# Optimization experiments

Hardware: AMD Instinct MI355X
Metric: run time of the kernel (lower is better)

## Reference

```python
import jax, jax.numpy as jnp
import numpy as np

B, S, HID = 1, 1024, 4096
NH, NKV, HD = 32, 8, 128
GROUPS = NH // NKV
THETA = 10000.0
SPAR = 0.5          # sparse_aggression (layer_idx > 0)
MIN_IDX = 4         # min_sparse_index: always-kept sink tokens
NEG = jnp.float32(-1e30)


def setup_inputs() -> dict:
    key = jax.random.key(0)
    k0, k1, k2, k3, k4 = jax.random.split(key, 5)
    sc = 0.02
    return {
        "hidden_states": jax.random.normal(k0, (B, S, HID), jnp.float32),
        "position_ids": jnp.arange(S, dtype=jnp.int32)[None, :],
        "Wq": jax.random.normal(k1, (NH * HD, HID), jnp.float32) * sc,
        "Wk": jax.random.normal(k2, (NKV * HD, HID), jnp.float32) * sc,
        "Wv": jax.random.normal(k3, (NKV * HD, HID), jnp.float32) * sc,
        "Wo": jax.random.normal(k4, (HID, NH * HD), jnp.float32) * sc,
    }


def _rotate_half(x):
    h = x.shape[-1] // 2
    return jnp.concatenate([-x[..., h:], x[..., :h]], axis=-1)


def _rope_cos_sin(position_ids):
    inv_freq = 1.0 / (THETA ** (jnp.arange(0, HD, 2, dtype=jnp.float32) / HD))
    freqs = position_ids.astype(jnp.float32)[..., None] * inv_freq  # [B,S,HD/2]
    emb = jnp.concatenate([freqs, freqs], axis=-1)                  # [B,S,HD]
    return jnp.cos(emb)[:, None], jnp.sin(emb)[:, None]             # [B,1,S,HD]


def reference(hidden_states, position_ids, Wq, Wk, Wv, Wo):
    b, s, _ = hidden_states.shape
    # QKV projections (nn.Linear: x @ W.T)
    q = (hidden_states @ Wq.T).reshape(b, s, NH, HD).transpose(0, 2, 1, 3)
    k = (hidden_states @ Wk.T).reshape(b, s, NKV, HD).transpose(0, 2, 1, 3)
    v = (hidden_states @ Wv.T).reshape(b, s, NKV, HD).transpose(0, 2, 1, 3)
    # RoPE
    cos, sin = _rope_cos_sin(position_ids)
    q = q * cos + _rotate_half(q) * sin
    k = k * cos + _rotate_half(k) * sin
    # repeat_kv (GQA expansion)
    k = jnp.repeat(k, GROUPS, axis=1)
    v = jnp.repeat(v, GROUPS, axis=1)
    # causal additive mask [1,1,S,S]
    causal = jnp.where(jnp.triu(jnp.ones((s, s), bool), 1), NEG, jnp.float32(0))[None, None]
    scale = 1.0 / np.sqrt(HD)
    scores = jnp.einsum('bhqd,bhkd->bhqk', q, k) * scale
    # oracle importance: softmax of (softmaxed) masked attention (no_grad in original)
    oracle = jax.nn.softmax((scores + causal).astype(jnp.float32), axis=-1)
    importance = jax.nn.softmax(oracle, axis=-1)
    importance = jax.lax.stop_gradient(importance)
    # descending sort -> rank of each key for each query
    sorted_idx = jnp.argsort(-importance, axis=-1)          # [B,H,S,S]
    ranks = jnp.argsort(sorted_idx, axis=-1)                # inverse perm
    # per-query token budget: keep ceil-ish top-k proportional to row length
    k_per_row = jnp.maximum((SPAR * (jnp.arange(s) + 1)).astype(jnp.int32), 1)
    key_idx = jnp.arange(s)
    kept = (ranks < k_per_row[None, None, :, None]) | (key_idx[None, None, None, :] < MIN_IDX)
    sparse_mask = jnp.where(kept, jnp.float32(0), NEG)
    # sparse attention
    attn = scores + sparse_mask + causal
    probs = jax.nn.softmax(attn.astype(jnp.float32), axis=-1).astype(v.dtype)
    out = jnp.einsum('bhqk,bhkd->bhqd', probs, v)           # [B,H,S,HD]
    out = out.transpose(0, 2, 1, 3).reshape(b, s, NH * HD)
    return out @ Wo.T
```

## Files before the change

kernel.cpp:

```cpp
#include <hip/hip_runtime.h>
#include <hip/hip_bf16.h>

#define S_LEN 1024
#define HID   4096
#define NH    32
#define NKV   8
#define HD    128
#define MIN_IDX 4
#define AO_COLS 4096
#define HEAD_STRIDE 131072

typedef __attribute__((ext_vector_type(8))) short short8;
typedef __attribute__((ext_vector_type(4))) float f32x4;

__device__ __forceinline__ unsigned short f2bf(float f) {
  union { float f; unsigned u; } v; v.f = f;
  unsigned r = v.u + 0x7FFFu + ((v.u >> 16) & 1u);
  return (unsigned short)(r >> 16);
}
__device__ __forceinline__ float bf2f(unsigned short h) {
  union { unsigned u; float f; } v; v.u = ((unsigned)h) << 16;
  return v.f;
}
__device__ __forceinline__ unsigned pk2(float a, float b) {
  union { __hip_bfloat162 h; unsigned u; } c;
  c.h = __float22bfloat162_rn(make_float2(a, b));
  return c.u;
}
__device__ __forceinline__ short8 pack8(float4 a, float4 b) {
  union { short8 s; unsigned u[4]; } r;
  r.u[0] = pk2(a.x, a.y); r.u[1] = pk2(a.z, a.w);
  r.u[2] = pk2(b.x, b.y); r.u[3] = pk2(b.z, b.w);
  return r.s;
}
__device__ __forceinline__ unsigned ordf(float f) {
  union { float f; int i; } v; v.f = f;
  return (unsigned)(v.i ^ ((v.i >> 31) | 0x80000000));
}
__device__ __forceinline__ float iordf(unsigned u) {
  union { int i; float f; } v;
  v.i = (u & 0x80000000u) ? (int)(u ^ 0x80000000u) : (int)~u;
  return v.f;
}
__device__ __forceinline__ float wave_sum_f(float v) {
  #pragma unroll
  for (int m = 32; m >= 1; m >>= 1) v += __shfl_xor(v, m);
  return v;
}
__device__ __forceinline__ unsigned wave_max_u(unsigned v) {
  #pragma unroll
  for (int m = 32; m >= 1; m >>= 1) { unsigned o = __shfl_xor(v, m); v = o > v ? o : v; }
  return v;
}
__device__ __forceinline__ void wave_lds_fence() {
  __builtin_amdgcn_s_waitcnt(0xC07F);
  __builtin_amdgcn_wave_barrier();
}
__device__ __forceinline__ void gload_lds16(const unsigned short* g, unsigned short* l) {
  auto gp = (const __attribute__((address_space(1))) unsigned*)g;
  auto lp = (__attribute__((address_space(3))) unsigned*)(unsigned)(unsigned long long)l;
  __builtin_amdgcn_global_load_lds(gp, lp, 16, 0, 0);
}

__global__ __launch_bounds__(256) void cvt4_k(
    const float* __restrict__ s0, const float* __restrict__ s1,
    const float* __restrict__ s2, const float* __restrict__ s3,
    unsigned short* __restrict__ d0, unsigned short* __restrict__ d1)
{
  const int b = blockIdx.x;
  const float* src; unsigned short* dst; int rb;
  if (b < 2048)       { src = s0; dst = d0;            rb = b; }
  else if (b < 10240) { src = s1; dst = d1;            rb = b - 2048; }
  else if (b < 12288) { src = s2; dst = d1 + 16777216; rb = b - 10240; }
  else                { src = s3; dst = d1 + 20971520; rb = b - 12288; }
  const size_t i = ((size_t)rb * 256 + threadIdx.x) * 8;
  float4 a = *(const float4*)(src + i);
  float4 c = *(const float4*)(src + i + 4);
  *(short8*)(dst + i) = pack8(a, c);
}

__global__ __launch_bounds__(256) void gemm_qkv_k(
    const unsigned short* __restrict__ Xb, const unsigned short* __restrict__ Wb,
    unsigned short* __restrict__ Qraw, unsigned short* __restrict__ Vt)
{
  __shared__ unsigned short As[3][128 * 32];
  __shared__ unsigned short Bs[3][128 * 32];
  const int nt = blockIdx.x;
  const int n0 = nt * 128;
  const int m0 = blockIdx.y * 128;
  const int t = threadIdx.x, w = t >> 6, lane = t & 63;
  const int wm = w >> 1, wn = w & 1;
  const int mcol = lane & 15, quad = lane >> 4;
  const int lrow = lane >> 2, lcol = (lane & 3) * 8;

  const unsigned short* Ag = Xb + (size_t)m0 * HID;
  const unsigned short* Bg = Wb + (size_t)n0 * HID;

  f32x4 acc[4][4];
  #pragma unroll
  for (int i = 0; i < 4; i++)
    #pragma unroll
    for (int j = 0; j < 4; j++) acc[i][j] = (f32x4){0.f, 0.f, 0.f, 0.f};

  constexpr int NT = HID / 32;
  #define STAGE_QKV(buf, k0)                                                  \
    { const int c0 = w * 2, c1 = w * 2 + 1;                                   \
      gload_lds16(Ag + (size_t)(c0*16 + lrow) * HID + (k0) + lcol, &As[buf][c0 * 512]); \
      gload_lds16(Bg + (size_t)(c0*16 + lrow) * HID + (k0) + lcol, &Bs[buf][c0 * 512]); \
      gload_lds16(Ag + (size_t)(c1*16 + lrow) * HID + (k0) + lcol, &As[buf][c1 * 512]); \
      gload_lds16(Bg + (size_t)(c1*16 + lrow) * HID + (k0) + lcol, &Bs[buf][c1 * 512]); }

  STAGE_QKV(0, 0)
  STAGE_QKV(1, 32)
  asm volatile("s_waitcnt vmcnt(4)" ::: "memory");
  __builtin_amdgcn_s_barrier();
  __builtin_amdgcn_sched_barrier(0);

  int cur = 0, stg = 2;
  for (int kt = 0; kt < NT; ++kt) {
    if (kt + 2 < NT) STAGE_QKV(stg, (kt + 2) * 32)
    short8 af[4], bf[4];
    #pragma unroll
    for (int i = 0; i < 4; i++) af[i] = *(const short8*)&As[cur][(wm*64 + i*16 + mcol)*32 + quad*8];
    #pragma unroll
    for (int j = 0; j < 4; j++) bf[j] = *(const short8*)&Bs[cur][(wn*64 + j*16 + mcol)*32 + quad*8];
    #pragma unroll
    for (int i = 0; i < 4; i++)
      #pragma unroll
      for (int j = 0; j < 4; j++)
        acc[i][j] = __builtin_amdgcn_mfma_f32_16x16x32_bf16(af[i], bf[j], acc[i][j], 0, 0, 0);
    if (kt + 2 < NT) { asm volatile("s_waitcnt vmcnt(4)" ::: "memory"); }
    else             { asm volatile("s_waitcnt vmcnt(0)" ::: "memory"); }
    __builtin_amdgcn_s_barrier();
    __builtin_amdgcn_sched_barrier(0);
    cur = (cur == 2) ? 0 : cur + 1;
    stg = (stg == 2) ? 0 : stg + 1;
  }

  if (nt < 40) {
    unsigned short* dst = Qraw + (size_t)nt * HEAD_STRIDE;
    #pragma unroll
    for (int i = 0; i < 4; i++) {
      const int rb = m0 + wm*64 + i*16 + quad*4;
      #pragma unroll
      for (int j = 0; j < 4; j++) {
        const int d = wn*64 + j*16 + mcol;
        #pragma unroll
        for (int r = 0; r < 4; r++)
          dst[(size_t)(rb + r) * HD + d] = f2bf(acc[i][j][r]);
      }
    }
  } else {
    unsigned short* dst = Vt + (size_t)(nt - 40) * HEAD_STRIDE;
    #pragma unroll
    for (int i = 0; i < 4; i++) {
      const int rb = m0 + wm*64 + i*16 + quad*4;
      #pragma unroll
      for (int j = 0; j < 4; j++) {
        const int d = wn*64 + j*16 + mcol;
        ushort4 v4;
        v4.x = f2bf(acc[i][j][0]); v4.y = f2bf(acc[i][j][1]);
        v4.z = f2bf(acc[i][j][2]); v4.w = f2bf(acc[i][j][3]);
        *(ushort4*)(dst + (size_t)d * S_LEN + rb) = v4;
      }
    }
  }
}

__global__ __launch_bounds__(256) void rope_qk_k(
    const int* __restrict__ pos_ids, unsigned short* __restrict__ Qraw)
{
  const int w = threadIdx.x >> 6, lane = threadIdx.x & 63;
  const int gw = blockIdx.x * 4 + w;
  const int hidx = gw >> 10;
  const int s = gw & 1023;
  const float pos = (float)pos_ids[s];
  const float invf = exp2f((float)lane * -0.20762050593045f);
  float sn, cs;
  sincosf(pos * invf, &sn, &cs);
  unsigned short* base = Qraw + (size_t)hidx * HEAD_STRIDE + (size_t)s * HD;
  const float x0 = bf2f(base[lane]), x1 = bf2f(base[lane + 64]);
  base[lane]      = f2bf(x0 * cs - x1 * sn);
  base[lane + 64] = f2bf(x1 * cs + x0 * sn);
}

#define SROW 1042
#define PSTR 2084

#define PROC_ROW(UARR, RR, LL, PRE, PM, KRM, TTT)                             \
  {                                                                           \
    const int r_ = (RR);                                                      \
    const int L_ = (LL);                                                      \
    unsigned btau = (PRE);                                                    \
    unsigned bmsk = (PM);                                                     \
    int kr = (KRM);                                                           \
    int tt = (TTT);                                                           \
    const int bs = (bmsk == 0u) ? 31 : (__builtin_ctz(bmsk) - 1);             \
    _Pragma("unroll 1")                                                       \
    for (int b = bs; b >= 0; --b) {                                           \
      if (tt <= kr) break;                                                    \
      const unsigned bit = 1u << b;                                           \
      const unsigned am = bmsk | bit;                                         \
      const unsigned test = btau | bit;                                       \
      int cnt = 0;                                                            \
      _Pragma("unroll")                                                       \
      for (int c = 0; c < NC; c++) {                                          \
        const int j = c * 64 + lane;                                          \
        cnt += (int)__popcll(__ballot(j < L_ && ((UARR)[c] & am) == test));   \
      }                                                                       \
      if (cnt >= kr) { btau = test; tt = cnt; }                               \
      else           { kr -= cnt; tt -= cnt; }                                \
      bmsk = am;                                                              \
    }                                                                         \
    unsigned um = 0;                                                          \
    _Pragma("unroll")                                                         \
    for (int c = 0; c < NC; c++) {                                            \
      const int j = c * 64 + lane;                                            \
      if (j < L_ && (UARR)[c] > um) um = (UARR)[c];                           \
    }                                                                         \
    const float mx = iordf(wave_max_u(um));                                   \
    float ssum = 0.f;                                                         \
    if (tt <= kr) {                                                           \
           \
      _Pragma("unroll")                                                       \
      for (int c = 0; c < NC; c++) {                                          \
        const int j = c * 64 + lane;                                          \
        const unsigned u = (UARR)[c];                                         \
        const bool kept = (j < L_) && ((u >= btau) || (j < MIN_IDX));         \
        const float e = kept ? __expf(iordf(u) - mx) : 0.f;                   \
        Pl[r_][c*64 + lane] = f2bf(e);                                        \
        ssum += e;                                                            \
      }                                                                       \
    } else {                                                                  \
      int tiebase = 0;                                                        \
      _Pragma("unroll")                                                       \
      for (int c = 0; c < NC; c++) {                                          \
        const int j = c * 64 + lane;                                          \
        const unsigned u = (UARR)[c];                                         \
        const unsigned umv = u & bmsk;                                        \
        const bool eq = (j < L_) && (umv == btau);                            \
        const unsigned long long bal = __ballot(eq);                          \
        const int trank = tiebase + (int)__popcll(bal & lmlt);                \
        tiebase += (int)__popcll(bal);                                        \
        const bool kept = (j < L_) &&                                         \
            ((umv > btau) || (eq && trank < kr) || (j < MIN_IDX));            \
        const float e = kept ? __expf(iordf(u) - mx) : 0.f;                   \
        Pl[r_][c*64 + lane] = f2bf(e);                                        \
        ssum += e;                                                            \
      }                                                                       \
    }                                                                         \
    ssum = wave_sum_f(ssum);                                                  \
    if (lane == 0) rowinv[r_] = 1.f / fmaxf(ssum, 1e-30f);                    \
  }

template<int KT>
__device__ __forceinline__ void attn_body(
    const unsigned short* __restrict__ Qb, const unsigned short* __restrict__ Kh,
    const unsigned short* __restrict__ Vh, unsigned short* __restrict__ AO,
    float (*S)[SROW], unsigned (*hist)[256], float* rowinv,
    int q0, int h, int w, int lane, int mcol, int quad)
{
  constexpr int NC = 2 * KT;
  const float scale = 0.08838834764831845f;
  unsigned short (*Pl)[PSTR] = (unsigned short (*)[PSTR])&S[0][0];
  const int wk = w & 3, wp = w >> 2;

  short8 aq[4];
  {
    const unsigned short* qrow = Qb + ((size_t)h * S_LEN + q0 + mcol) * HD + quad * 8;
    #pragma unroll
    for (int kk = 0; kk < 4; kk++) aq[kk] = *(const short8*)(qrow + kk * 32);
  }

  #pragma unroll
  for (int kt = wp; kt < KT; kt += 2) {
    short8 bfr[2][4];
    #pragma unroll
    for (int g2 = 0; g2 < 2; g2++) {
      const int key = kt * 128 + (wk * 2 + g2) * 16 + mcol;
      const unsigned short* krow = Kh + (size_t)key * HD + quad * 8;
      #pragma unroll
      for (int kk = 0; kk < 4; kk++) bfr[g2][kk] = *(const short8*)(krow + kk * 32);
    }
    f32x4 d4[2];
    d4[0] = (f32x4){0.f,0.f,0.f,0.f}; d4[1] = (f32x4){0.f,0.f,0.f,0.f};
    #pragma unroll
    for (int g2 = 0; g2 < 2; g2++)
      #pragma unroll
      for (int kk = 0; kk < 4; kk++)
        d4[g2] = __builtin_amdgcn_mfma_f32_16x16x32_bf16(aq[kk], bfr[g2][kk], d4[g2], 0, 0, 0);
    #pragma unroll
    for (int g2 = 0; g2 < 2; g2++) {
      const int ckey = kt * 128 + (wk * 2 + g2) * 16 + mcol;
      #pragma unroll
      for (int r = 0; r < 4; r++) S[quad*4 + r][ckey] = d4[g2][r] * scale;
    }
  }
  __syncthreads();

  const unsigned long long lmlt = (1ull << lane) - 1ull;
  const int rep = lane & 3;
  {
    const int ra = w * 2, rbn = ra + 1;
    const int L0 = q0 + ra + 1, L1 = q0 + rbn + 1;
    unsigned u0[NC], u1[NC];
    #pragma unroll
    for (int c = 0; c < NC; c++) {
      u0[c] = ordf(S[ra][c*64 + lane]);
      u1[c] = ordf(S[rbn][c*64 + lane]);
    }
    int ks0 = L0 >> 1; if (ks0 < 1) ks0 = 1;
    int ks1 = L1 >> 1; if (ks1 < 1) ks1 = 1;
    int krem0 = ks0, tot0 = L0, krem1 = ks1, tot1 = L1;
    unsigned pre0 = 0u, pre1 = 0u, pm0 = 0u, pm1 = 0u;

    #pragma unroll
    for (int pass = 0; pass < 3; pass++) {
      const int shift = 26 - pass * 6;
      const bool a0 = tot0 > krem0, a1 = tot1 > krem1;
      if (!a0 && !a1) continue;
      { uint4 z = {0u, 0u, 0u, 0u}; *(uint4*)&hist[w][lane * 4] = z; }
      wave_lds_fence();
      #pragma unroll
      for (int c = 0; c < NC; c++) {
        const int j = c * 64 + lane;
        if (a0 && j < L0 && (u0[c] & pm0) == pre0)
          atomicAdd(&hist[w][((u0[c] >> shift) & 63) * 4 + rep], 1u);
        if (a1 && j < L1 && (u1[c] & pm1) == pre1)
          atomicAdd(&hist[w][((u1[c] >> shift) & 63) * 4 + rep], 1u << 16);
      }
      wave_lds_fence();
      const uint4 cv = *(const uint4*)&hist[w][(63 - lane) * 4];
      const unsigned cnt2 = cv.x + cv.y + cv.z + cv.w;
      unsigned x = cnt2;
      #pragma unroll
      for (int d2 = 1; d2 < 64; d2 <<= 1) { unsigned y = __shfl_up(x, d2); if (lane >= d2) x += y; }
      const unsigned runp = x - cnt2;
      if (a0) {
        const int run = (int)(runp & 0xFFFFu);
        const int cn  = (int)(cnt2 & 0xFFFFu);
        const bool hit = (run < krem0) && (run + cn >= krem0);
        unsigned packv = hit ? (((unsigned)(63 - lane) << 22) |
                                ((unsigned)run << 11) | (unsigned)cn) : 0u;
        const unsigned long long bal = __ballot(hit);
        const int srcl = __ffsll(bal) - 1;
        const unsigned res = __shfl(packv, srcl);
        krem0 -= (int)((res >> 11) & 0x7FF);
        tot0 = (int)(res & 0x7FF);
        pre0 |= ((unsigned)(res >> 22)) << shift;
        pm0 |= 63u << shift;
      }
      if (a1) {
        const int run = (int)(runp >> 16);
        const int cn  = (int)(cnt2 >> 16);
        const bool hit = (run < krem1) && (run + cn >= krem1);
        unsigned packv = hit ? (((unsigned)(63 - lane) << 22) |
                                ((unsigned)run << 11) | (unsigned)cn) : 0u;
        const unsigned long long bal = __ballot(hit);
        const int srcl = __ffsll(bal) - 1;
        const unsigned res = __shfl(packv, srcl);
        krem1 -= (int)((res >> 11) & 0x7FF);
        tot1 = (int)(res & 0x7FF);
        pre1 |= ((unsigned)(res >> 22)) << shift;
        pm1 |= 63u << shift;
      }
    }
    PROC_ROW(u0, ra,  L0, pre0, pm0, krem0, tot0)
    PROC_ROW(u1, rbn, L1, pre1, pm1, krem1, tot1)
  }
  __syncthreads();

  f32x4 opv = (f32x4){0.f,0.f,0.f,0.f};
  const int d = w * 16 + mcol;
  #pragma unroll
  for (int kt = 0; kt < KT; kt++) {
    #pragma unroll
    for (int kb = 0; kb < 4; kb++) {
      short8 af = *(const short8*)&Pl[mcol][kt*128 + kb*32 + quad*8];
      short8 bfr = *(const short8*)(Vh + (size_t)d * S_LEN + kt*128 + kb*32 + quad*8);
      opv = __builtin_amdgcn_mfma_f32_16x16x32_bf16(af, bfr, opv, 0, 0, 0);
    }
  }
  {
    const int col = h * HD + d;
    #pragma unroll
    for (int r2 = 0; r2 < 4; r2++) {
      const int row = q0 + quad*4 + r2;
      AO[(size_t)row * AO_COLS + col] = f2bf(opv[r2] * rowinv[quad*4 + r2]);
    }
  }
}

__global__ __launch_bounds__(512, 4) void attn_k(
    const unsigned short* __restrict__ Qb, const unsigned short* __restrict__ Kb,
    const unsigned short* __restrict__ Vt, unsigned short* __restrict__ AO,
    const float* __restrict__ WoF, unsigned short* __restrict__ Wob)
{
  __shared__ float S[16][SROW];
  __shared__ unsigned hist[8][256];
  __shared__ float rowinv[16];
  const int bid = (int)blockIdx.x;
  if (bid >= 2048) {
    const size_t i = ((size_t)(bid - 2048) * 512 + threadIdx.x) * 8;
    float4 a = *(const float4*)(WoF + i);
    float4 c = *(const float4*)(WoF + i + 4);
    *(short8*)(Wob + i) = pack8(a, c);
    return;
  }
  const int bx = bid & 63;
  const int h = bid >> 6;
  const int rb = 63 - bx;
  const int kvh = h >> 2;
  const int q0 = rb * 16;
  const int kt_max = (rb >> 3) + 1;
  const int t = threadIdx.x, w = t >> 6, lane = t & 63;
  const int mcol = lane & 15, quad = lane >> 4;
  const unsigned short* Kh = Kb + (size_t)kvh * HEAD_STRIDE;
  const unsigned short* Vh = Vt + (size_t)kvh * HEAD_STRIDE;

  switch (kt_max) {
    case 1: attn_body<1>(Qb, Kh, Vh, AO, S, hist, rowinv, q0, h, w, lane, mcol, quad); break;
    case 2: attn_body<2>(Qb, Kh, Vh, AO, S, hist, rowinv, q0, h, w, lane, mcol, quad); break;
    case 3: attn_body<3>(Qb, Kh, Vh, AO, S, hist, rowinv, q0, h, w, lane, mcol, quad); break;
    case 4: attn_body<4>(Qb, Kh, Vh, AO, S, hist, rowinv, q0, h, w, lane, mcol, quad); break;
    case 5: attn_body<5>(Qb, Kh, Vh, AO, S, hist, rowinv, q0, h, w, lane, mcol, quad); break;
    case 6: attn_body<6>(Qb, Kh, Vh, AO, S, hist, rowinv, q0, h, w, lane, mcol, quad); break;
    case 7: attn_body<7>(Qb, Kh, Vh, AO, S, hist, rowinv, q0, h, w, lane, mcol, quad); break;
    default: attn_body<8>(Qb, Kh, Vh, AO, S, hist, rowinv, q0, h, w, lane, mcol, quad); break;
  }
}

__global__ __launch_bounds__(256) void gemm_out_k(
    const unsigned short* __restrict__ A, const unsigned short* __restrict__ Wob,
    float* __restrict__ Out)
{
  __shared__ unsigned short As[3][128 * 32];
  __shared__ unsigned short Bs[3][128 * 32];
  const int n0 = blockIdx.x * 128;
  const int m0 = blockIdx.y * 128;
  const int kbase = blockIdx.z * 2048;
  const int t = threadIdx.x, w = t >> 6, lane = t & 63;
  const int wm = w >> 1, wn = w & 1;
  const int mcol = lane & 15, quad = lane >> 4;
  const int lrow = lane >> 2, lcol = (lane & 3) * 8;

  const unsigned short* Ag = A   + (size_t)m0 * AO_COLS + kbase;
  const unsigned short* Bg = Wob + (size_t)n0 * AO_COLS + kbase;

  f32x4 acc[4][4];
  #pragma unroll
  for (int i = 0; i < 4; i++)
    #pragma unroll
    for (int j = 0; j < 4; j++) acc[i][j] = (f32x4){0.f, 0.f, 0.f, 0.f};

  constexpr int NT = 2048 / 32;
  #define STAGE_OUT(buf, k0)                                                  \
    { const int c0 = w * 2, c1 = w * 2 + 1;                                   \
      gload_lds16(Ag + (size_t)(c0*16 + lrow) * AO_COLS + (k0) + lcol, &As[buf][c0 * 512]); \
      gload_lds16(Bg + (size_t)(c0*16 + lrow) * AO_COLS + (k0) + lcol, &Bs[buf][c0 * 512]); \
      gload_lds16(Ag + (size_t)(c1*16 + lrow) * AO_COLS + (k0) + lcol, &As[buf][c1 * 512]); \
      gload_lds16(Bg + (size_t)(c1*16 + lrow) * AO_COLS + (k0) + lcol, &Bs[buf][c1 * 512]); }

  STAGE_OUT(0, 0)
  STAGE_OUT(1, 32)
  asm volatile("s_waitcnt vmcnt(4)" ::: "memory");
  __builtin_amdgcn_s_barrier();
  __builtin_amdgcn_sched_barrier(0);

  int cur = 0, stg = 2;
  for (int kt = 0; kt < NT; ++kt) {
    if (kt + 2 < NT) STAGE_OUT(stg, (kt + 2) * 32)
    short8 af[4], bf[4];
    #pragma unroll
    for (int i = 0; i < 4; i++) af[i] = *(const short8*)&As[cur][(wm*64 + i*16 + mcol)*32 + quad*8];
    #pragma unroll
    for (int j = 0; j < 4; j++) bf[j] = *(const short8*)&Bs[cur][(wn*64 + j*16 + mcol)*32 + quad*8];
    #pragma unroll
    for (int i = 0; i < 4; i++)
      #pragma unroll
      for (int j = 0; j < 4; j++)
        acc[i][j] = __builtin_amdgcn_mfma_f32_16x16x32_bf16(af[i], bf[j], acc[i][j], 0, 0, 0);
    if (kt + 2 < NT) { asm volatile("s_waitcnt vmcnt(4)" ::: "memory"); }
    else             { asm volatile("s_waitcnt vmcnt(0)" ::: "memory"); }
    __builtin_amdgcn_s_barrier();
    __builtin_amdgcn_sched_barrier(0);
    cur = (cur == 2) ? 0 : cur + 1;
    stg = (stg == 2) ? 0 : stg + 1;
  }

  #pragma unroll
  for (int i = 0; i < 4; i++) {
    const int rb = m0 + wm*64 + i*16 + quad*4;
    #pragma unroll
    for (int j = 0; j < 4; j++) {
      const int col = n0 + wn*64 + j*16 + mcol;
      #pragma unroll
      for (int r = 0; r < 4; r++)
        atomicAdd(&Out[(size_t)(rb + r) * HID + col], acc[i][j][r]);
    }
  }
}

extern "C" void kernel_launch(void* const* d_in, const int* in_sizes, int n_in,
                              void* d_out, int out_size, void* d_ws, size_t ws_size,
                              hipStream_t stream) {
  (void)in_sizes; (void)n_in; (void)out_size; (void)ws_size;
  const float* X   = (const float*)d_in[0];
  const int*   pos = (const int*)d_in[1];
  const float* Wq  = (const float*)d_in[2];
  const float* Wk  = (const float*)d_in[3];
  const float* Wv  = (const float*)d_in[4];
  const float* Wo  = (const float*)d_in[5];
  float* out = (float*)d_out;

  char* ws = (char*)d_ws;
  unsigned short* Qraw  = (unsigned short*)ws;
  unsigned short* Kraw  = (unsigned short*)(ws + 8388608);
  unsigned short* Vt    = (unsigned short*)(ws + 10485760);
  unsigned short* AO    = (unsigned short*)(ws + 12582912);
  unsigned short* Xb    = (unsigned short*)(ws + 20971520);
  unsigned short* Wqkvb = (unsigned short*)(ws + 29360128);
  unsigned short* Wob   = Wqkvb;

  cvt4_k<<<dim3(14336), dim3(256), 0, stream>>>(X, Wq, Wk, Wv, Xb, Wqkvb);

  gemm_qkv_k<<<dim3(48, 8),  dim3(256), 0, stream>>>(Xb, Wqkvb, Qraw, Vt);
  rope_qk_k <<<dim3(10240),  dim3(256), 0, stream>>>(pos, Qraw);

  hipMemsetAsync(out, 0, (size_t)S_LEN * HID * sizeof(float), stream);

  attn_k    <<<dim3(6144),   dim3(512), 0, stream>>>(Qraw, Kraw, Vt, AO, Wo, Wob);
  gemm_out_k<<<dim3(32, 8, 2), dim3(256), 0, stream>>>(AO, Wob, out);
}
```

Measured before the change: 446.6 us.

## Split-K the Q/K projection GEMM with fp32 atomic accumulation

The QKV GEMM now splits the Q and K column tiles into two K-halves, launching 88 column blocks instead of 48 so more workgroups run concurrently. Partial sums go into an fp32 scratch buffer (borrowing the output and AO regions) via atomicAdd, and the RoPE kernel reads that fp32 buffer and writes bf16 Q/K. V tiles keep the full-K path with direct transposed stores. This raises occupancy on a grid that was smaller than the CU count, at the cost of extra memsets, atomic traffic and an fp32 round trip.

```diff
diff --git a/kernel.cpp b/kernel.cpp
--- a/kernel.cpp
+++ b/kernel.cpp
@@ -9,6 +9,7 @@
 #define MIN_IDX 4
 #define AO_COLS 4096
 #define HEAD_STRIDE 131072
+#define P32_SPLIT 4194304
 
 typedef __attribute__((ext_vector_type(8))) short short8;
 typedef __attribute__((ext_vector_type(4))) float f32x4;
@@ -60,6 +61,9 @@
   auto gp = (const __attribute__((address_space(1))) unsigned*)g;
   auto lp = (__attribute__((address_space(3))) unsigned*)(unsigned)(unsigned long long)l;
   __builtin_amdgcn_global_load_lds(gp, lp, 16, 0, 0);
+}
+__device__ __forceinline__ float* p32ptr(float* outp, float* aof, size_t e) {
+  return (e < (size_t)P32_SPLIT) ? (outp + e) : (aof + (e - P32_SPLIT));
 }
 
 __global__ __launch_bounds__(256) void cvt4_k(
@@ -81,11 +85,17 @@
 
 __global__ __launch_bounds__(256) void gemm_qkv_k(
     const unsigned short* __restrict__ Xb, const unsigned short* __restrict__ Wb,
-    unsigned short* __restrict__ Qraw, unsigned short* __restrict__ Vt)
+    float* __restrict__ P32a, float* __restrict__ P32b,
+    unsigned short* __restrict__ Vt)
 {
   __shared__ unsigned short As[3][128 * 32];
   __shared__ unsigned short Bs[3][128 * 32];
-  const int nt = blockIdx.x;
+  const int x = blockIdx.x;
+  const bool isV = x < 8;
+  int nt, kbase, ntiles;
+  if (isV) { nt = 40 + x;            kbase = 0;                 ntiles = 128; }
+  else     { const int idx = x - 8;  nt = idx >> 1;
+             kbase = (idx & 1) * 2048;                          ntiles = 64;  }
   const int n0 = nt * 128;
   const int m0 = blockIdx.y * 128;
   const int t = threadIdx.x, w = t >> 6, lane = t & 63;
@@ -93,8 +103,8 @@
   const int mcol = lane & 15, quad = lane >> 4;
   const int lrow = lane >> 2, lcol = (lane & 3) * 8;
 
-  const unsigned short* Ag = Xb + (size_t)m0 * HID;
-  const unsigned short* Bg = Wb + (size_t)n0 * HID;
+  const unsigned short* Ag = Xb + (size_t)m0 * HID + kbase;
+  const unsigned short* Bg = Wb + (size_t)n0 * HID + kbase;
 
   f32x4 acc[4][4];
   #pragma unroll
@@ -102,7 +112,6 @@
     #pragma unroll
     for (int j = 0; j < 4; j++) acc[i][j] = (f32x4){0.f, 0.f, 0.f, 0.f};
 
-  constexpr int NT = HID / 32;
   #define STAGE_QKV(buf, k0)                                                  \
     { const int c0 = w * 2, c1 = w * 2 + 1;                                   \
       gload_lds16(Ag + (size_t)(c0*16 + lrow) * HID + (k0) + lcol, &As[buf][c0 * 512]); \
@@ -117,8 +126,8 @@
   __builtin_amdgcn_sched_barrier(0);
 
   int cur = 0, stg = 2;
-  for (int kt = 0; kt < NT; ++kt) {
-    if (kt + 2 < NT) STAGE_QKV(stg, (kt + 2) * 32)
+  for (int kt = 0; kt < ntiles; ++kt) {
+    if (kt + 2 < ntiles) STAGE_QKV(stg, (kt + 2) * 32)
     short8 af[4], bf[4];
     #pragma unroll
     for (int i = 0; i < 4; i++) af[i] = *(const short8*)&As[cur][(wm*64 + i*16 + mcol)*32 + quad*8];
@@ -129,28 +138,15 @@
       #pragma unroll
       for (int j = 0; j < 4; j++)
         acc[i][j] = __builtin_amdgcn_mfma_f32_16x16x32_bf16(af[i], bf[j], acc[i][j], 0, 0, 0);
-    if (kt + 2 < NT) { asm volatile("s_waitcnt vmcnt(4)" ::: "memory"); }
-    else             { asm volatile("s_waitcnt vmcnt(0)" ::: "memory"); }
+    if (kt + 2 < ntiles) { asm volatile("s_waitcnt vmcnt(4)" ::: "memory"); }
+    else                 { asm volatile("s_waitcnt vmcnt(0)" ::: "memory"); }
     __builtin_amdgcn_s_barrier();
     __builtin_amdgcn_sched_barrier(0);
     cur = (cur == 2) ? 0 : cur + 1;
     stg = (stg == 2) ? 0 : stg + 1;
   }
 
-  if (nt < 40) {
-    unsigned short* dst = Qraw + (size_t)nt * HEAD_STRIDE;
-    #pragma unroll
-    for (int i = 0; i < 4; i++) {
-      const int rb = m0 + wm*64 + i*16 + quad*4;
-      #pragma unroll
-      for (int j = 0; j < 4; j++) {
-        const int d = wn*64 + j*16 + mcol;
-        #pragma unroll
-        for (int r = 0; r < 4; r++)
-          dst[(size_t)(rb + r) * HD + d] = f2bf(acc[i][j][r]);
-      }
-    }
-  } else {
+  if (isV) {
     unsigned short* dst = Vt + (size_t)(nt - 40) * HEAD_STRIDE;
     #pragma unroll
     for (int i = 0; i < 4; i++) {
@@ -164,11 +160,25 @@
         *(ushort4*)(dst + (size_t)d * S_LEN + rb) = v4;
       }
     }
+  } else {
+    #pragma unroll
+    for (int i = 0; i < 4; i++) {
+      const int rb = m0 + wm*64 + i*16 + quad*4;
+      #pragma unroll
+      for (int j = 0; j < 4; j++) {
+        const int nc = n0 + wn*64 + j*16 + mcol;
+        #pragma unroll
+        for (int r = 0; r < 4; r++)
+          atomicAdd(p32ptr(P32a, P32b, (size_t)(rb + r) * 5120 + nc), acc[i][j][r]);
+      }
+    }
   }
 }
 
 __global__ __launch_bounds__(256) void rope_qk_k(
-    const int* __restrict__ pos_ids, unsigned short* __restrict__ Qraw)
+    const int* __restrict__ pos_ids,
+    const float* __restrict__ P32a, const float* __restrict__ P32b,
+    unsigned short* __restrict__ Qraw)
 {
   const int w = threadIdx.x >> 6, lane = threadIdx.x & 63;
   const int gw = blockIdx.x * 4 + w;
@@ -178,8 +188,10 @@
   const float invf = exp2f((float)lane * -0.20762050593045f);
   float sn, cs;
   sincosf(pos * invf, &sn, &cs);
+  const size_t e0 = (size_t)s * 5120 + (size_t)hidx * 128 + lane;
+  const float x0 = *p32ptr((float*)P32a, (float*)P32b, e0);
+  const float x1 = *p32ptr((float*)P32a, (float*)P32b, e0 + 64);
   unsigned short* base = Qraw + (size_t)hidx * HEAD_STRIDE + (size_t)s * HD;
-  const float x0 = bf2f(base[lane]), x1 = bf2f(base[lane + 64]);
   base[lane]      = f2bf(x0 * cs - x1 * sn);
   base[lane + 64] = f2bf(x1 * cs + x0 * sn);
 }
@@ -518,14 +530,18 @@
   unsigned short* Kraw  = (unsigned short*)(ws + 8388608);
   unsigned short* Vt    = (unsigned short*)(ws + 10485760);
   unsigned short* AO    = (unsigned short*)(ws + 12582912);
+  float*          AOf   = (float*)AO;
   unsigned short* Xb    = (unsigned short*)(ws + 20971520);
   unsigned short* Wqkvb = (unsigned short*)(ws + 29360128);
   unsigned short* Wob   = Wqkvb;
 
   cvt4_k<<<dim3(14336), dim3(256), 0, stream>>>(X, Wq, Wk, Wv, Xb, Wqkvb);
 
-  gemm_qkv_k<<<dim3(48, 8),  dim3(256), 0, stream>>>(Xb, Wqkvb, Qraw, Vt);
-  rope_qk_k <<<dim3(10240),  dim3(256), 0, stream>>>(pos, Qraw);
+  hipMemsetAsync(out, 0, (size_t)P32_SPLIT * sizeof(float), stream);
+  hipMemsetAsync(AOf, 0, 4194304, stream);
+
+  gemm_qkv_k<<<dim3(88, 8),  dim3(256), 0, stream>>>(Xb, Wqkvb, out, AOf, Vt);
+  rope_qk_k <<<dim3(10240),  dim3(256), 0, stream>>>(pos, out, AOf, Qraw);
 
   hipMemsetAsync(out, 0, (size_t)S_LEN * HID * sizeof(float), stream);
 
```

Result: slower. 495.7 us (+11.0%).
